# Optimization experiments

Measured on AMD Instinct MI355X. Metric: run time of the kernel, lower is better.

Reference implementation:

```python
import jax, jax.numpy as jnp
import numpy as np

N_NODES = 100000
N_EDGES = 3200000
N_FEAT = 512
N_DIMS = 256
N_CLSS = 10


def setup_inputs() -> dict:
    key = jax.random.key(0)
    ks = jax.random.split(key, 9)
    x = jax.random.normal(ks[0], (N_NODES, N_FEAT), dtype=jnp.float32)
    edge_index = jax.random.randint(ks[1], (2, N_EDGES), 0, N_NODES, dtype=jnp.int64)
    edge_weight = jax.random.uniform(ks[2], (N_EDGES,), dtype=jnp.float32)
    # GCNConv params (glorot-ish scale)
    W1 = jax.random.normal(ks[3], (N_FEAT, N_DIMS), dtype=jnp.float32) / np.sqrt(N_FEAT)
    b1 = jnp.zeros((N_DIMS,), dtype=jnp.float32)
    W2 = jax.random.normal(ks[4], (N_DIMS, N_DIMS), dtype=jnp.float32) / np.sqrt(N_DIMS)
    b2 = jnp.zeros((N_DIMS,), dtype=jnp.float32)
    Wc = jax.random.normal(ks[5], (N_DIMS, N_CLSS), dtype=jnp.float32) / np.sqrt(N_DIMS)
    bc = jnp.zeros((N_CLSS,), dtype=jnp.float32)
    return {"x": x, "edge_index": edge_index, "edge_weight": edge_weight,
            "W1": W1, "b1": b1, "W2": W2, "b2": b2, "Wc": Wc, "bc": bc}


def _gcn_norm(edge_index, edge_weight, num_nodes):
    # Add self-loops with weight 1 (PyG GCNConv default, add_self_loops=True)
    loop = jnp.arange(num_nodes, dtype=edge_index.dtype)
    row = jnp.concatenate([edge_index[0], loop])
    col = jnp.concatenate([edge_index[1], loop])
    w = jnp.concatenate([edge_weight, jnp.ones((num_nodes,), dtype=edge_weight.dtype)])
    deg = jax.ops.segment_sum(w, col, num_segments=num_nodes)
    dinv = jnp.where(deg > 0, jax.lax.rsqrt(deg), 0.0)
    norm = dinv[row] * w * dinv[col]  # D^-1/2 A D^-1/2
    return row, col, norm


def _gcn_conv(x, row, col, norm, W, b, num_nodes):
    h = x @ W                                 # [N, d_out]
    msg = norm[:, None] * h[row]              # gather + scale  [E+N, d_out]
    out = jax.ops.segment_sum(msg, col, num_segments=num_nodes)  # scatter-add
    return out + b


def reference(x, edge_index, edge_weight, W1, b1, W2, b2, Wc, bc):
    n = x.shape[0]
    row, col, norm = _gcn_norm(edge_index, edge_weight, n)
    h = _gcn_conv(x, row, col, norm, W1, b1, n)
    h = jax.nn.relu(h)  # dropout is identity in eval mode
    h = _gcn_conv(h, row, col, norm, W2, b2, n)
    h = jax.nn.relu(h)
    return h @ Wc + bc  # args.task == 0 -> linear classifier
```

## Files before the change

### kernel.cpp

```cpp
#include <hip/hip_runtime.h>


__global__ __launch_bounds__(256) void init_kernel(float* deg, int* cnt, int* cur, int N) {
    int i = blockIdx.x * 256 + threadIdx.x;
    if (i < N) { deg[i] = 1.0f; cnt[i] = 0; cur[i] = 0; }
}

__global__ __launch_bounds__(256) void deg_cnt_kernel(const int* __restrict__ col,
                                                      const float* __restrict__ w,
                                                      float* deg, int* cnt, int E) {
    int e = blockIdx.x * 256 + threadIdx.x;
    if (e < E) {
        int c = col[e];
        atomicAdd(&deg[c], w[e]);
        atomicAdd(&cnt[c], 1);
    }
}

__global__ __launch_bounds__(256) void dinv_kernel(float* deg, int N) {
    int i = blockIdx.x * 256 + threadIdx.x;
    if (i < N) deg[i] = rsqrtf(deg[i]);
}

__global__ __launch_bounds__(1024) void scan_kernel(const int* __restrict__ cnt,
                                                    int* __restrict__ off, int N) {
    __shared__ int sm[1024];
    int t = threadIdx.x;
    int chunk = (N + 1023) >> 10;
    int b = t * chunk;
    int e = min(b + chunk, N);
    int s = 0;
    for (int i = b; i < e; i++) s += cnt[i];
    sm[t] = s;
    __syncthreads();
#pragma unroll
    for (int d = 1; d < 1024; d <<= 1) {
        int v = (t >= d) ? sm[t - d] : 0;
        __syncthreads();
        sm[t] += v;
        __syncthreads();
    }
    int run = sm[t] - s;
    for (int i = b; i < e; i++) { off[i] = run; run += cnt[i]; }
    if (t == 1023) off[N] = sm[1023];
}

__global__ __launch_bounds__(256) void fill_kernel(const int* __restrict__ row,
                                                   const int* __restrict__ col,
                                                   const float* __restrict__ w,
                                                   const float* __restrict__ dinv,
                                                   const int* __restrict__ off, int* cur,
                                                   int* __restrict__ csr_r,
                                                   float* __restrict__ csr_n, int E) {
    int e = blockIdx.x * 256 + threadIdx.x;
    if (e >= E) return;
    int r = row[e], c = col[e];
    int pos = off[c] + atomicAdd(&cur[c], 1);
    csr_r[pos] = r;
    csr_n[pos] = dinv[r] * w[e] * dinv[c];
}

__global__ __launch_bounds__(256) void gemm_kernel(const float* __restrict__ A,
                                                   const float* __restrict__ B,
                                                   float* __restrict__ C,
                                                   int M, int N, int K) {
    __shared__ float As[16][64];
    __shared__ float Bs[16][64];
    int t  = threadIdx.x;
    int tx = t & 15, ty = t >> 4;
    int row0 = blockIdx.x * 64, col0 = blockIdx.y * 64;
    float acc[4][4] = {};

    int ar = t >> 2, ac = (t & 3) << 2;
    int br = t >> 4, bc = (t & 15) << 2;
    bool aval = (row0 + ar) < M;
    const float* Ap = A + (size_t)(row0 + ar) * K + ac;
    const float* Bp = B + (size_t)br * N + col0 + bc;

    for (int k0 = 0; k0 < K; k0 += 16) {
        float4 a4 = make_float4(0.f, 0.f, 0.f, 0.f);
        if (aval) a4 = *(const float4*)(Ap + k0);
        float4 b4 = *(const float4*)(Bp + (size_t)k0 * N);
        As[ac + 0][ar] = a4.x; As[ac + 1][ar] = a4.y;
        As[ac + 2][ar] = a4.z; As[ac + 3][ar] = a4.w;
        *(float4*)&Bs[br][bc] = b4;
        __syncthreads();
#pragma unroll
        for (int k = 0; k < 16; k++) {
            float4 av = *(const float4*)&As[k][ty << 2];
            float4 bv = *(const float4*)&Bs[k][tx << 2];
            acc[0][0] += av.x * bv.x; acc[0][1] += av.x * bv.y; acc[0][2] += av.x * bv.z; acc[0][3] += av.x * bv.w;
            acc[1][0] += av.y * bv.x; acc[1][1] += av.y * bv.y; acc[1][2] += av.y * bv.z; acc[1][3] += av.y * bv.w;
            acc[2][0] += av.z * bv.x; acc[2][1] += av.z * bv.y; acc[2][2] += av.z * bv.z; acc[2][3] += av.z * bv.w;
            acc[3][0] += av.w * bv.x; acc[3][1] += av.w * bv.y; acc[3][2] += av.w * bv.z; acc[3][3] += av.w * bv.w;
        }
        __syncthreads();
    }
#pragma unroll
    for (int i = 0; i < 4; i++) {
        int r = row0 + (ty << 2) + i;
        if (r < M)
            *(float4*)&C[(size_t)r * N + col0 + (tx << 2)] =
                make_float4(acc[i][0], acc[i][1], acc[i][2], acc[i][3]);
    }
}

__global__ __launch_bounds__(256) void agg_kernel(const float* __restrict__ h,
                                                  const int* __restrict__ csr_r,
                                                  const float* __restrict__ csr_n,
                                                  const int* __restrict__ off,
                                                  const float* __restrict__ dinv,
                                                  const float* __restrict__ bias,
                                                  float* __restrict__ out, int N, int relu) {
    int lane = threadIdx.x & 63;
    int n = blockIdx.x * 4 + (threadIdx.x >> 6);
    if (n >= N) return;
    n = __builtin_amdgcn_readfirstlane(n);
    int start = off[n], end = off[n + 1];
    float d = dinv[n];
    const float4* hv = (const float4*)h;
    float4 self = hv[(size_t)n * 64 + lane];
    float sw = d * d;
    float ax = sw * self.x, ay = sw * self.y, az = sw * self.z, aw = sw * self.w;
    int j = start;
    for (; j + 4 <= end; j += 4) {
        int r0 = csr_r[j], r1 = csr_r[j + 1], r2 = csr_r[j + 2], r3 = csr_r[j + 3];
        float n0 = csr_n[j], n1 = csr_n[j + 1], n2 = csr_n[j + 2], n3 = csr_n[j + 3];
        float4 h0 = hv[(size_t)r0 * 64 + lane];
        float4 h1 = hv[(size_t)r1 * 64 + lane];
        float4 h2 = hv[(size_t)r2 * 64 + lane];
        float4 h3 = hv[(size_t)r3 * 64 + lane];
        ax += n0 * h0.x + n1 * h1.x + n2 * h2.x + n3 * h3.x;
        ay += n0 * h0.y + n1 * h1.y + n2 * h2.y + n3 * h3.y;
        az += n0 * h0.z + n1 * h1.z + n2 * h2.z + n3 * h3.z;
        aw += n0 * h0.w + n1 * h1.w + n2 * h2.w + n3 * h3.w;
    }
    for (; j < end; j++) {
        int r = csr_r[j];
        float nm = csr_n[j];
        float4 hr = hv[(size_t)r * 64 + lane];
        ax += nm * hr.x; ay += nm * hr.y; az += nm * hr.z; aw += nm * hr.w;
    }
    float4 b = ((const float4*)bias)[lane];
    ax += b.x; ay += b.y; az += b.z; aw += b.w;
    if (relu) {
        ax = fmaxf(ax, 0.f); ay = fmaxf(ay, 0.f);
        az = fmaxf(az, 0.f); aw = fmaxf(aw, 0.f);
    }
    ((float4*)out)[(size_t)n * 64 + lane] = make_float4(ax, ay, az, aw);
}

__global__ __launch_bounds__(256) void cls_kernel(const float* __restrict__ h,
                                                  const float* __restrict__ Wc,
                                                  const float* __restrict__ bc,
                                                  float* __restrict__ out, int N) {
    __shared__ float Ws[256 * 10];
    for (int i = threadIdx.x; i < 2560; i += 256) Ws[i] = Wc[i];
    __syncthreads();
    int lane = threadIdx.x & 63;
    int n = blockIdx.x * 4 + (threadIdx.x >> 6);
    if (n >= N) return;
    float4 hv4 = ((const float4*)h)[(size_t)n * 64 + lane];
    float s[10];
#pragma unroll
    for (int c = 0; c < 10; c++) {
        float v = hv4.x * Ws[(4 * lane + 0) * 10 + c] + hv4.y * Ws[(4 * lane + 1) * 10 + c] +
                  hv4.z * Ws[(4 * lane + 2) * 10 + c] + hv4.w * Ws[(4 * lane + 3) * 10 + c];
#pragma unroll
        for (int m = 32; m; m >>= 1) v += __shfl_xor(v, m, 64);
        s[c] = v;
    }
    float outv = 0.0f;
#pragma unroll
    for (int c = 0; c < 10; c++)
        if (lane == c) outv = s[c] + bc[c];
    if (lane < 10) out[(size_t)n * 10 + lane] = outv;
}

extern "C" void kernel_launch(void* const* d_in, const int* in_sizes, int n_in,
                              void* d_out, int out_size, void* d_ws, size_t ws_size,
                              hipStream_t stream) {
    const float* x  = (const float*)d_in[0];
    const int*   ei = (const int*)d_in[1];
    const float* ew = (const float*)d_in[2];
    const float* W1 = (const float*)d_in[3];
    const float* b1 = (const float*)d_in[4];
    const float* W2 = (const float*)d_in[5];
    const float* b2 = (const float*)d_in[6];
    const float* Wc = (const float*)d_in[7];
    const float* bc = (const float*)d_in[8];
    float* out = (float*)d_out;

    const int E = in_sizes[1] / 2;
    const int F = 512, D = 256;
    const int N = in_sizes[0] / F;
    const int* row = ei;
    const int* col = ei + E;

    char* ws = (char*)d_ws;
    size_t p = 0;
    auto alloc = [&](size_t bytes) -> char* {
        char* r = ws + p;
        p += (bytes + 255) & ~(size_t)255;
        return r;
    };
    float* deg   = (float*)alloc((size_t)N * 4);
    int*   off   = (int*)alloc((size_t)(N + 1) * 4);
    int*   cnt   = (int*)alloc((size_t)N * 4);
    int*   cur   = (int*)alloc((size_t)N * 4);
    int*   csr_r = (int*)alloc((size_t)E * 4);
    float* csr_n = (float*)alloc((size_t)E * 4);
    float* h     = (float*)alloc((size_t)N * D * 4);
    float* agg   = (float*)alloc((size_t)N * D * 4);
    (void)ws_size;

    init_kernel<<<(N + 255) / 256, 256, 0, stream>>>(deg, cnt, cur, N);
    deg_cnt_kernel<<<(E + 255) / 256, 256, 0, stream>>>(col, ew, deg, cnt, E);
    dinv_kernel<<<(N + 255) / 256, 256, 0, stream>>>(deg, N);
    scan_kernel<<<1, 1024, 0, stream>>>(cnt, off, N);
    fill_kernel<<<(E + 255) / 256, 256, 0, stream>>>(row, col, ew, deg, off, cur, csr_r, csr_n, E);

    dim3 gg((N + 63) / 64, D / 64);
    gemm_kernel<<<gg, 256, 0, stream>>>(x, W1, h, N, D, F);
    agg_kernel<<<(N + 3) / 4, 256, 0, stream>>>(h, csr_r, csr_n, off, deg, b1, agg, N, 1);
    gemm_kernel<<<gg, 256, 0, stream>>>(agg, W2, h, N, D, D);
    agg_kernel<<<(N + 3) / 4, 256, 0, stream>>>(h, csr_r, csr_n, off, deg, b2, agg, N, 1);
    cls_kernel<<<(N + 3) / 4, 256, 0, stream>>>(agg, Wc, bc, out, N);
}
```

Before: 2.526 ms.

## Replace FP32 SIMT GEMMs with split-FP16 MFMA GEMMs using prepacked weights

Replaces the shared-memory FP32 tiled GEMM with an MFMA kernel. Each FP32 operand is split into high and low FP16 parts, and three 16x16x32 FP16 MFMAs per tile recover near-FP32 accuracy. Weights are split and repacked into a k-interleaved FP16 layout by a new prep kernel, and each wave computes a 16x256 output strip with A read directly from global memory and no LDS. This trades exact FP32 arithmetic and extra weight-prep launches for matrix-core throughput. The output width is hard-coded to 256.

Result: faster. 2.381 ms (-5.8%).

```diff
diff --git a/kernel.cpp b/kernel.cpp
--- a/kernel.cpp
+++ b/kernel.cpp
@@ -1,5 +1,8 @@
 #include <hip/hip_runtime.h>
 
+
+typedef __attribute__((ext_vector_type(8))) _Float16 f16x8;
+typedef __attribute__((ext_vector_type(4))) float f32x4;
 
 __global__ __launch_bounds__(256) void init_kernel(float* deg, int* cnt, int* cur, int N) {
     int i = blockIdx.x * 256 + threadIdx.x;
@@ -60,48 +63,78 @@
     csr_n[pos] = dinv[r] * w[e] * dinv[c];
 }
 
-__global__ __launch_bounds__(256) void gemm_kernel(const float* __restrict__ A,
-                                                   const float* __restrict__ B,
-                                                   float* __restrict__ C,
-                                                   int M, int N, int K) {
-    __shared__ float As[16][64];
-    __shared__ float Bs[16][64];
-    int t  = threadIdx.x;
-    int tx = t & 15, ty = t >> 4;
-    int row0 = blockIdx.x * 64, col0 = blockIdx.y * 64;
-    float acc[4][4] = {};
-
-    int ar = t >> 2, ac = (t & 3) << 2;
-    int br = t >> 4, bc = (t & 15) << 2;
-    bool aval = (row0 + ar) < M;
-    const float* Ap = A + (size_t)(row0 + ar) * K + ac;
-    const float* Bp = B + (size_t)br * N + col0 + bc;
-
-    for (int k0 = 0; k0 < K; k0 += 16) {
-        float4 a4 = make_float4(0.f, 0.f, 0.f, 0.f);
-        if (aval) a4 = *(const float4*)(Ap + k0);
-        float4 b4 = *(const float4*)(Bp + (size_t)k0 * N);
-        As[ac + 0][ar] = a4.x; As[ac + 1][ar] = a4.y;
-        As[ac + 2][ar] = a4.z; As[ac + 3][ar] = a4.w;
-        *(float4*)&Bs[br][bc] = b4;
-        __syncthreads();
-#pragma unroll
-        for (int k = 0; k < 16; k++) {
-            float4 av = *(const float4*)&As[k][ty << 2];
-            float4 bv = *(const float4*)&Bs[k][tx << 2];
-            acc[0][0] += av.x * bv.x; acc[0][1] += av.x * bv.y; acc[0][2] += av.x * bv.z; acc[0][3] += av.x * bv.w;
-            acc[1][0] += av.y * bv.x; acc[1][1] += av.y * bv.y; acc[1][2] += av.y * bv.z; acc[1][3] += av.y * bv.w;
-            acc[2][0] += av.z * bv.x; acc[2][1] += av.z * bv.y; acc[2][2] += av.z * bv.z; acc[2][3] += av.z * bv.w;
-            acc[3][0] += av.w * bv.x; acc[3][1] += av.w * bv.y; acc[3][2] += av.w * bv.z; acc[3][3] += av.w * bv.w;
+__global__ __launch_bounds__(256) void prep_b_kernel(const float* __restrict__ B,
+                                                     _Float16* __restrict__ Bph,
+                                                     _Float16* __restrict__ Bpl, int K) {
+    int e = blockIdx.x * 256 + threadIdx.x;
+    if (e >= K * 256) return;
+    int k = e >> 8, n = e & 255;
+    float v = B[e];
+    _Float16 h = (_Float16)v;
+    _Float16 lo = (_Float16)(v - (float)h);
+    size_t idx = ((((size_t)(k >> 3)) * 256 + n) << 3) | (k & 7);
+    Bph[idx] = h;
+    Bpl[idx] = lo;
+}
+
+__global__ __launch_bounds__(256) void gemm_split_kernel(const float* __restrict__ A,
+                                                         const _Float16* __restrict__ Bph,
+                                                         const _Float16* __restrict__ Bpl,
+                                                         float* __restrict__ C,
+                                                         int M, int K) {
+    int t = threadIdx.x;
+    int w = t >> 6, l = t & 63;
+    int lr = l & 15;
+    int lg = l >> 4;
+    int m0 = blockIdx.x * 64 + w * 16;
+
+    int arow = m0 + lr;
+    if (arow >= M) arow = M - 1;
+    const float* Ap = A + (size_t)arow * K + lg * 8;
+
+    f32x4 acc[16];
+#pragma unroll
+    for (int i = 0; i < 16; i++) acc[i] = (f32x4)0.0f;
+
+    const f16x8* BH = (const f16x8*)Bph;
+    const f16x8* BL = (const f16x8*)Bpl;
+
+    for (int k0 = 0; k0 < K; k0 += 64) {
+#pragma unroll
+        for (int ks = 0; ks < 2; ks++) {
+            const float* ap = Ap + k0 + ks * 32;
+            f32x4 a0 = *(const f32x4*)ap;
+            f32x4 a1 = *(const f32x4*)(ap + 4);
+            f16x8 ah, al;
+#pragma unroll
+            for (int j = 0; j < 4; j++) {
+                float v = a0[j];
+                _Float16 hi = (_Float16)v;
+                ah[j] = hi;
+                al[j] = (_Float16)(v - (float)hi);
+                float v2 = a1[j];
+                _Float16 hi2 = (_Float16)v2;
+                ah[j + 4] = hi2;
+                al[j + 4] = (_Float16)(v2 - (float)hi2);
+            }
+            size_t bbase = ((size_t)(((k0 + ks * 32) >> 3) + lg)) * 256 + lr;
+#pragma unroll
+            for (int nf = 0; nf < 16; nf++) {
+                f16x8 bh = BH[bbase + nf * 16];
+                f16x8 bl = BL[bbase + nf * 16];
+                acc[nf] = __builtin_amdgcn_mfma_f32_16x16x32_f16(ah, bh, acc[nf], 0, 0, 0);
+                acc[nf] = __builtin_amdgcn_mfma_f32_16x16x32_f16(al, bh, acc[nf], 0, 0, 0);
+                acc[nf] = __builtin_amdgcn_mfma_f32_16x16x32_f16(ah, bl, acc[nf], 0, 0, 0);
+            }
         }
-        __syncthreads();
-    }
-#pragma unroll
-    for (int i = 0; i < 4; i++) {
-        int r = row0 + (ty << 2) + i;
-        if (r < M)
-            *(float4*)&C[(size_t)r * N + col0 + (tx << 2)] =
-                make_float4(acc[i][0], acc[i][1], acc[i][2], acc[i][3]);
+    }
+#pragma unroll
+    for (int nf = 0; nf < 16; nf++) {
+#pragma unroll
+        for (int r = 0; r < 4; r++) {
+            int row = m0 + lg * 4 + r;
+            if (row < M) C[(size_t)row * 256 + nf * 16 + lr] = acc[nf][r];
+        }
     }
 }
 
@@ -212,6 +245,10 @@
     float* csr_n = (float*)alloc((size_t)E * 4);
     float* h     = (float*)alloc((size_t)N * D * 4);
     float* agg   = (float*)alloc((size_t)N * D * 4);
+    _Float16* Bp1h = (_Float16*)alloc((size_t)F * D * 2);
+    _Float16* Bp1l = (_Float16*)alloc((size_t)F * D * 2);
+    _Float16* Bp2h = (_Float16*)alloc((size_t)D * D * 2);
+    _Float16* Bp2l = (_Float16*)alloc((size_t)D * D * 2);
     (void)ws_size;
 
     init_kernel<<<(N + 255) / 256, 256, 0, stream>>>(deg, cnt, cur, N);
@@ -220,10 +257,13 @@
     scan_kernel<<<1, 1024, 0, stream>>>(cnt, off, N);
     fill_kernel<<<(E + 255) / 256, 256, 0, stream>>>(row, col, ew, deg, off, cur, csr_r, csr_n, E);
 
-    dim3 gg((N + 63) / 64, D / 64);
-    gemm_kernel<<<gg, 256, 0, stream>>>(x, W1, h, N, D, F);
+    prep_b_kernel<<<(F * D + 255) / 256, 256, 0, stream>>>(W1, Bp1h, Bp1l, F);
+    prep_b_kernel<<<(D * D + 255) / 256, 256, 0, stream>>>(W2, Bp2h, Bp2l, D);
+
+    int gm = (N + 63) / 64;
+    gemm_split_kernel<<<gm, 256, 0, stream>>>(x, Bp1h, Bp1l, h, N, F);
     agg_kernel<<<(N + 3) / 4, 256, 0, stream>>>(h, csr_r, csr_n, off, deg, b1, agg, N, 1);
-    gemm_kernel<<<gg, 256, 0, stream>>>(agg, W2, h, N, D, D);
+    gemm_split_kernel<<<gm, 256, 0, stream>>>(agg, Bp2h, Bp2l, h, N, D);
     agg_kernel<<<(N + 3) / 4, 256, 0, stream>>>(h, csr_r, csr_n, off, deg, b2, agg, N, 1);
     cls_kernel<<<(N + 3) / 4, 256, 0, stream>>>(agg, Wc, bc, out, N);
 }
```
